# Optimization experiments

Measured on AMD Instinct MI355X. Metric: run time of the kernel, lower is better.

The kernel has to match this reference:

```python
import jax, jax.numpy as jnp
import numpy as np

N_NODES = 50000
N_EDGES = 400000
DIMS = [128, 256, 512, 256, 64, 2]


def setup_inputs() -> dict:
    key = jax.random.key(0)
    ks = jax.random.split(key, 16)
    x = jax.random.normal(ks[0], (N_NODES, DIMS[0]), dtype=jnp.float32)
    edge_index = jax.random.randint(ks[1], (2, N_EDGES), 0, N_NODES, dtype=jnp.int64)
    inp = {"x": x, "edge_index": edge_index}
    for i in range(5):
        fan_in, fan_out = DIMS[i], DIMS[i + 1]
        scale = (2.0 / (fan_in + fan_out)) ** 0.5  # glorot-ish
        inp[f"W{i+1}"] = jax.random.normal(ks[2 + 2 * i], (fan_in, fan_out), dtype=jnp.float32) * scale
        inp[f"b{i+1}"] = jnp.zeros((fan_out,), dtype=jnp.float32)
    return inp


def _gcn_norm(edge_index, n):
    # add self-loops, compute symmetric normalization D^{-1/2} A_hat D^{-1/2}
    loop = jnp.arange(n, dtype=edge_index.dtype)
    src = jnp.concatenate([edge_index[0], loop])
    dst = jnp.concatenate([edge_index[1], loop])
    deg = jax.ops.segment_sum(jnp.ones_like(dst, dtype=jnp.float32), dst, num_segments=n)
    dinv = jnp.where(deg > 0, jax.lax.rsqrt(deg), 0.0)
    norm = dinv[src] * dinv[dst]  # [E+N]
    return src, dst, norm


def _gcn_conv(h, W, b, src, dst, norm, n):
    h = h @ W                                   # [N, out]
    msg = h[src] * norm[:, None]                # gather + scale, [E+N, out]
    out = jax.ops.segment_sum(msg, dst, num_segments=n)  # scatter-add
    return out + b


def reference(x, edge_index, W1, b1, W2, b2, W3, b3, W4, b4, W5, b5):
    n = x.shape[0]
    src, dst, norm = _gcn_norm(edge_index, n)
    h = jax.nn.relu(_gcn_conv(x, W1, b1, src, dst, norm, n))
    h = jax.nn.relu(_gcn_conv(h, W2, b2, src, dst, norm, n))
    h = jax.nn.relu(_gcn_conv(h, W3, b3, src, dst, norm, n))
    h = jax.nn.relu(_gcn_conv(h, W4, b4, src, dst, norm, n))
    h = _gcn_conv(h, W5, b5, src, dst, norm, n)
    return jax.nn.log_softmax(h, axis=1)
```

## Files before the change

kernel.cpp:

```cpp
#include <hip/hip_runtime.h>
#include <math.h>

#define N_NODES 50000
#define N_EDGES 400000

typedef __bf16 bf16x8 __attribute__((ext_vector_type(8)));
typedef float f32x4 __attribute__((ext_vector_type(4)));

__device__ __forceinline__ unsigned bf16_rne(float v) {
    unsigned u = __float_as_uint(v);
    return (u + 0x7FFFu + ((u >> 16) & 1u)) >> 16;
}
__device__ __forceinline__ unsigned pack_split(float v) {
    unsigned hi = bf16_rne(v);
    float hif = __uint_as_float(hi << 16);
    unsigned lo = bf16_rne(v - hif);
    return (hi << 16) | lo;
}
__device__ __forceinline__ float unpack_ps(unsigned w) {
    return __uint_as_float(w & 0xFFFF0000u) + __uint_as_float(w << 16);
}

__global__ void k_zero_i(int* __restrict__ p, int n) {
    int i = blockIdx.x * blockDim.x + threadIdx.x;
    if (i < n) p[i] = 0;
}

__global__ void k_count(const int* __restrict__ dst, int* __restrict__ cnt) {
    int e = blockIdx.x * blockDim.x + threadIdx.x;
    if (e < N_EDGES) atomicAdd(&cnt[dst[e]], 1);
}

__global__ __launch_bounds__(1024) void k_scan(const int* __restrict__ cnt,
                                               int* __restrict__ rowptr,
                                               float* __restrict__ dinv, int n) {
    __shared__ int sm[1024];
    __shared__ int carry;
    if (threadIdx.x == 0) carry = 0;
    __syncthreads();
    for (int base = 0; base < n; base += 1024) {
        int i = base + threadIdx.x;
        int v = (i < n) ? cnt[i] : 0;
        sm[threadIdx.x] = v;
        __syncthreads();
        for (int off = 1; off < 1024; off <<= 1) {
            int t = (threadIdx.x >= (unsigned)off) ? sm[threadIdx.x - off] : 0;
            __syncthreads();
            sm[threadIdx.x] += t;
            __syncthreads();
        }
        if (i < n) {
            rowptr[i] = carry + sm[threadIdx.x] - v;
            dinv[i] = rsqrtf((float)(v + 1));
        }
        __syncthreads();
        if (threadIdx.x == 0) carry += sm[1023];
        __syncthreads();
    }
    if (threadIdx.x == 0) rowptr[n] = carry;
}

__global__ void k_copy_i(const int* __restrict__ s, int* __restrict__ d, int n) {
    int i = blockIdx.x * blockDim.x + threadIdx.x;
    if (i < n) d[i] = s[i];
}

__global__ void k_fill(const int* __restrict__ src, const int* __restrict__ dst,
                       int* __restrict__ cursor, int* __restrict__ csr) {
    int e = blockIdx.x * blockDim.x + threadIdx.x;
    if (e >= N_EDGES) return;
    int d = dst[e];
    int pos = atomicAdd(&cursor[d], 1);
    csr[pos] = src[e];
}

__global__ void k_wprep(const float* __restrict__ W, unsigned* __restrict__ Wtp, int K, int N) {
    int i = blockIdx.x * blockDim.x + threadIdx.x;
    if (i >= K * N) return;
    int k = i / N, n = i % N;
    Wtp[(size_t)n * K + k] = pack_split(W[i]);
}

__global__ void k_rowscale(const float* __restrict__ x, const float* __restrict__ dinv,
                           float* __restrict__ xs) {
    int idx = blockIdx.x * blockDim.x + threadIdx.x;
    if (idx >= N_NODES * 32) return;
    int i = idx >> 5;
    float4 v = ((const float4*)x)[idx];
    float s = dinv[i];
    v.x *= s; v.y *= s; v.z *= s; v.w *= s;
    ((float4*)xs)[idx] = v;
}

template <int VEC, int MODE, int INP, int OUTP>
__global__ __launch_bounds__(256) void k_agg(
    const void* __restrict__ gv, const int* __restrict__ rowptr,
    const int* __restrict__ csr, const float* __restrict__ dinv,
    const float* __restrict__ bias, void* __restrict__ ov)
{
    constexpr int W = 64 * VEC;
    const int wave = threadIdx.x >> 6, lane = threadIdx.x & 63;
    const int node = blockIdx.x * 4 + wave;
    if (node >= N_NODES) return;
    const int col = lane * VEC;

    float acc[VEC];
#pragma unroll
    for (int v = 0; v < VEC; ++v) acc[v] = 0.f;

    auto fetch_add = [&](int r) {
        if constexpr (INP) {
            const unsigned* p = (const unsigned*)gv + (size_t)r * W + col;
            if constexpr (VEC == 4) {
                uint4 t = *(const uint4*)p;
                acc[0] += unpack_ps(t.x); acc[1] += unpack_ps(t.y);
                acc[2] += unpack_ps(t.z); acc[3] += unpack_ps(t.w);
            } else if constexpr (VEC == 2) {
                uint2 t = *(const uint2*)p;
                acc[0] += unpack_ps(t.x); acc[1] += unpack_ps(t.y);
            } else acc[0] += unpack_ps(*p);
        } else {
            const float* p = (const float*)gv + (size_t)r * W + col;
            if constexpr (VEC == 4) {
                float4 t = *(const float4*)p;
                acc[0] += t.x; acc[1] += t.y; acc[2] += t.z; acc[3] += t.w;
            } else if constexpr (VEC == 2) {
                float2 t = *(const float2*)p;
                acc[0] += t.x; acc[1] += t.y;
            } else acc[0] += *(const float*)p;
        }
    };

    fetch_add(node);
    const int beg = rowptr[node], end = rowptr[node + 1];
    for (int j = beg; j < end; ++j) fetch_add(csr[j]);

    const float sc = dinv[node];
    float r[VEC];
#pragma unroll
    for (int v = 0; v < VEC; ++v) {
        float t = sc * acc[v];
        if (MODE == 1) t = fmaxf(t + bias[col + v], 0.f);
        r[v] = t;
    }
    if constexpr (OUTP) {
        unsigned* po = (unsigned*)ov + (size_t)node * W + col;
        if constexpr (VEC == 4)
            *(uint4*)po = make_uint4(pack_split(r[0]), pack_split(r[1]), pack_split(r[2]), pack_split(r[3]));
        else if constexpr (VEC == 2)
            *(uint2*)po = make_uint2(pack_split(r[0]), pack_split(r[1]));
        else *po = pack_split(r[0]);
    } else {
        float* po = (float*)ov + (size_t)node * W + col;
        if constexpr (VEC == 4) *(float4*)po = make_float4(r[0], r[1], r[2], r[3]);
        else if constexpr (VEC == 2) *(float2*)po = make_float2(r[0], r[1]);
        else *po = r[0];
    }
}

__global__ void k_agg2(const float* __restrict__ g, const int* __restrict__ rowptr,
                       const int* __restrict__ csr, const float* __restrict__ dinv,
                       float* __restrict__ o) {
    int i = blockIdx.x * blockDim.x + threadIdx.x;
    if (i >= N_NODES) return;
    float2 a = *(const float2*)&g[2 * (size_t)i];
    int beg = rowptr[i], end = rowptr[i + 1];
    for (int j = beg; j < end; ++j) {
        int s = csr[j];
        float2 t = *(const float2*)&g[2 * (size_t)s];
        a.x += t.x; a.y += t.y;
    }
    float sc = dinv[i];
    o[2 * (size_t)i + 0] = sc * a.x;
    o[2 * (size_t)i + 1] = sc * a.y;
}

__global__ __launch_bounds__(256) void k_gemm_mfma(
    const unsigned* __restrict__ Ap, const unsigned* __restrict__ Wtp,
    const float* __restrict__ dinv, const float* __restrict__ bias,
    unsigned* __restrict__ Gp, int M, int K, int N, int mode)
{
    __shared__ char lds[24576];
    char* Ahi = lds;
    char* Alo = lds + 8192;
    char* Bhi = lds + 16384;
    char* Blo = lds + 20480;

    const int tid = threadIdx.x;
    const int m0 = blockIdx.x * 128;
    const int n0 = blockIdx.y * 64;
    const int wv = tid >> 6, l = tid & 63;
    const int lr = l & 15, ls = l >> 4;

    int aoff[2], boff[4];
#pragma unroll
    for (int h = 0; h < 2; ++h) {
        int row = wv * 32 + h * 16 + lr;
        aoff[h] = (row * 64 + ls * 16) ^ ((row & 7) << 4);
    }
#pragma unroll
    for (int j = 0; j < 4; ++j) {
        int row = j * 16 + lr;
        boff[j] = (row * 64 + ls * 16) ^ ((row & 7) << 4);
    }

    f32x4 acc[2][4] = {};

    for (int kt = 0; kt < K; kt += 32) {
        __syncthreads();
#pragma unroll
        for (int p = 0; p < 4; ++p) {
            int c = p * 256 + tid;
            int row = c >> 3, c4 = (c & 7) * 4;
            int grow = m0 + row;
            uint4 w = make_uint4(0u, 0u, 0u, 0u);
            if (grow < M) w = *(const uint4*)&Ap[(size_t)grow * K + kt + c4];
            ushort4 hi, lo;
            hi.x = w.x >> 16; lo.x = w.x & 0xFFFFu;
            hi.y = w.y >> 16; lo.y = w.y & 0xFFFFu;
            hi.z = w.z >> 16; lo.z = w.z & 0xFFFFu;
            hi.w = w.w >> 16; lo.w = w.w & 0xFFFFu;
            int off = (row * 64 + c4 * 2) ^ ((row & 7) << 4);
            *(ushort4*)(Ahi + off) = hi;
            *(ushort4*)(Alo + off) = lo;
        }
#pragma unroll
        for (int p = 0; p < 2; ++p) {
            int c = p * 256 + tid;
            int row = c >> 3, c4 = (c & 7) * 4;
            uint4 w = *(const uint4*)&Wtp[(size_t)(n0 + row) * K + kt + c4];
            ushort4 hi, lo;
            hi.x = w.x >> 16; lo.x = w.x & 0xFFFFu;
            hi.y = w.y >> 16; lo.y = w.y & 0xFFFFu;
            hi.z = w.z >> 16; lo.z = w.z & 0xFFFFu;
            hi.w = w.w >> 16; lo.w = w.w & 0xFFFFu;
            int off = (row * 64 + c4 * 2) ^ ((row & 7) << 4);
            *(ushort4*)(Bhi + off) = hi;
            *(ushort4*)(Blo + off) = lo;
        }
        __syncthreads();

        bf16x8 ah[2], al[2], bh[4], bl[4];
#pragma unroll
        for (int h = 0; h < 2; ++h) {
            ah[h] = *(const bf16x8*)(Ahi + aoff[h]);
            al[h] = *(const bf16x8*)(Alo + aoff[h]);
        }
#pragma unroll
        for (int j = 0; j < 4; ++j) {
            bh[j] = *(const bf16x8*)(Bhi + boff[j]);
            bl[j] = *(const bf16x8*)(Blo + boff[j]);
        }
#pragma unroll
        for (int h = 0; h < 2; ++h)
#pragma unroll
            for (int j = 0; j < 4; ++j) {
                acc[h][j] = __builtin_amdgcn_mfma_f32_16x16x32_bf16(ah[h], bh[j], acc[h][j], 0, 0, 0);
                acc[h][j] = __builtin_amdgcn_mfma_f32_16x16x32_bf16(ah[h], bl[j], acc[h][j], 0, 0, 0);
                acc[h][j] = __builtin_amdgcn_mfma_f32_16x16x32_bf16(al[h], bh[j], acc[h][j], 0, 0, 0);
            }
    }

#pragma unroll
    for (int h = 0; h < 2; ++h)
#pragma unroll
        for (int j = 0; j < 4; ++j) {
            int col = n0 + j * 16 + lr;
            float bc = (mode >= 1) ? bias[col] : 0.f;
#pragma unroll
            for (int reg = 0; reg < 4; ++reg) {
                int r = m0 + wv * 32 + h * 16 + ls * 4 + reg;
                if (r < M) {
                    float t = acc[h][j][reg];
                    if (mode == 0)      t = dinv[r] * t;
                    else if (mode == 1) t = fmaxf(t + bc, 0.f);
                    else                t = dinv[r] * fmaxf(t + bc, 0.f);
                    Gp[(size_t)r * N + col] = pack_split(t);
                }
            }
        }
}

__global__ void k_gemm2(const float* __restrict__ A, const float* __restrict__ W,
                        const float* __restrict__ dinv, float* __restrict__ G, int M, int K)
{
    int i = blockIdx.x * blockDim.x + threadIdx.x;
    if (i >= M) return;
    float a0 = 0.f, a1 = 0.f;
    for (int k = 0; k < K; k += 4) {
        float4 a = *(const float4*)&A[(size_t)i * K + k];
        a0 += a.x * W[(k + 0) * 2 + 0] + a.y * W[(k + 1) * 2 + 0]
            + a.z * W[(k + 2) * 2 + 0] + a.w * W[(k + 3) * 2 + 0];
        a1 += a.x * W[(k + 0) * 2 + 1] + a.y * W[(k + 1) * 2 + 1]
            + a.z * W[(k + 2) * 2 + 1] + a.w * W[(k + 3) * 2 + 1];
    }
    float s = dinv[i];
    G[2 * (size_t)i + 0] = s * a0;
    G[2 * (size_t)i + 1] = s * a1;
}

__global__ void k_final(const float* __restrict__ lg, const float* __restrict__ bias,
                        float* __restrict__ out, int M)
{
    int i = blockIdx.x * blockDim.x + threadIdx.x;
    if (i >= M) return;
    float o0 = lg[2 * (size_t)i + 0] + bias[0];
    float o1 = lg[2 * (size_t)i + 1] + bias[1];
    float m = fmaxf(o0, o1);
    float lse = m + logf(expf(o0 - m) + expf(o1 - m));
    out[2 * (size_t)i + 0] = o0 - lse;
    out[2 * (size_t)i + 1] = o1 - lse;
}

extern "C" void kernel_launch(void* const* d_in, const int* in_sizes, int n_in,
                              void* d_out, int out_size, void* d_ws, size_t ws_size,
                              hipStream_t stream) {
    const float* x   = (const float*)d_in[0];
    const int*   ei  = (const int*)d_in[1];
    const int*   src = ei;
    const int*   dst = ei + N_EDGES;
    const float* W1 = (const float*)d_in[2];  const float* b1 = (const float*)d_in[3];
    const float* W2 = (const float*)d_in[4];  const float* b2 = (const float*)d_in[5];
    const float* W3 = (const float*)d_in[6];  const float* b3 = (const float*)d_in[7];
    const float* W4 = (const float*)d_in[8];  const float* b4 = (const float*)d_in[9];
    const float* W5 = (const float*)d_in[10]; const float* b5 = (const float*)d_in[11];
    float* out = (float*)d_out;

    char* ws = (char*)d_ws;
    float*    dinv   = (float*)(ws + 0);
    int*      cnt    = (int*)(ws + 256 * 1024);
    int*      rowptr = (int*)(ws + 512 * 1024);
    int*      cursor = (int*)(ws + 768 * 1024);
    int*      csr    = (int*)(ws + 1024 * 1024);
    unsigned* wt1 = (unsigned*)(ws + 3 * 1024 * 1024);
    unsigned* wt2 = wt1 + 128 * 256;
    unsigned* wt3 = wt2 + 256 * 512;
    unsigned* wt4 = wt3 + 512 * 256;

    char* D = ws + 6 * 1024 * 1024;
    float*    xs   = (float*)D;
    unsigned* aggx = (unsigned*)(D + (size_t)N_NODES * 128 * 4);
    unsigned* h1s  = (unsigned*)(D + (size_t)N_NODES * 512 * 4);
    unsigned* a2   = (unsigned*)(D + (size_t)N_NODES * 768 * 4);
    unsigned* h2   = (unsigned*)D;
    unsigned* g3s  = h1s;
    unsigned* h3   = a2;
    unsigned* g4s  = (unsigned*)D;
    float*    h4   = (float*)(D + (size_t)N_NODES * 64 * 4);
    float*    g5s  = (float*)(D + (size_t)N_NODES * 128 * 4);
    float*    lgt  = (float*)(D + (size_t)N_NODES * 132 * 4);

    const int T = 256;
    const int nodeB = (N_NODES + T - 1) / T;
    const int edgeB = (N_EDGES + T - 1) / T;
    const int aggB  = (N_NODES + 3) / 4;
    const int gx    = (N_NODES + 127) / 128;

    k_zero_i<<<nodeB, T, 0, stream>>>(cnt, N_NODES);
    k_count<<<edgeB, T, 0, stream>>>(dst, cnt);
    k_scan<<<1, 1024, 0, stream>>>(cnt, rowptr, dinv, N_NODES);
    k_copy_i<<<nodeB, T, 0, stream>>>(rowptr, cursor, N_NODES);
    k_fill<<<edgeB, T, 0, stream>>>(src, dst, cursor, csr);
    k_wprep<<<(128 * 256 + T - 1) / T, T, 0, stream>>>(W1, wt1, 128, 256);
    k_wprep<<<(256 * 512 + T - 1) / T, T, 0, stream>>>(W2, wt2, 256, 512);
    k_wprep<<<(512 * 256 + T - 1) / T, T, 0, stream>>>(W3, wt3, 512, 256);
    k_wprep<<<(256 * 64 + T - 1) / T, T, 0, stream>>>(W4, wt4, 256, 64);

    k_rowscale<<<(N_NODES * 32 + T - 1) / T, T, 0, stream>>>(x, dinv, xs);
    k_agg<2, 0, 0, 1><<<aggB, T, 0, stream>>>(xs, rowptr, csr, dinv, nullptr, aggx);
    k_gemm_mfma<<<dim3(gx, 4), T, 0, stream>>>(aggx, wt1, dinv, b1, h1s, N_NODES, 128, 256, 2);

    k_agg<4, 0, 1, 1><<<aggB, T, 0, stream>>>(h1s, rowptr, csr, dinv, nullptr, a2);
    k_gemm_mfma<<<dim3(gx, 8), T, 0, stream>>>(a2, wt2, dinv, b2, h2, N_NODES, 256, 512, 1);

    k_gemm_mfma<<<dim3(gx, 4), T, 0, stream>>>(h2, wt3, dinv, nullptr, g3s, N_NODES, 512, 256, 0);
    k_agg<4, 1, 1, 1><<<aggB, T, 0, stream>>>(g3s, rowptr, csr, dinv, b3, h3);

    k_gemm_mfma<<<dim3(gx, 1), T, 0, stream>>>(h3, wt4, dinv, nullptr, g4s, N_NODES, 256, 64, 0);
    k_agg<1, 1, 1, 0><<<aggB, T, 0, stream>>>(g4s, rowptr, csr, dinv, b4, h4);

    k_gemm2<<<nodeB, T, 0, stream>>>(h4, W5, dinv, g5s, N_NODES, 64);
    k_agg2<<<nodeB, T, 0, stream>>>(g5s, rowptr, csr, dinv, lgt);
    k_final<<<nodeB, T, 0, stream>>>(lgt, b5, out, N_NODES);
}
```

Measured before the change: 747.3 us.

## Template MFMA GEMM on 2x2 wave grid with larger N tiles

The split-bf16 MFMA GEMM becomes a template over per-wave tile sizes, and its four waves are arranged as a 2x2 grid instead of stacking along M. Blocks now cover 128x128 output tiles (128x64 for the last layer), which halves the number of blocks re-reading the A operand per row tile and raises arithmetic intensity per LDS load. The grid axes are swapped so column tiles vary fastest, letting blocks that share the same A rows run close together for L2 reuse. In exchange each wave holds more accumulators (4x4 fragments), which raises register pressure and may lower occupancy, and the larger tiles mean fewer blocks in flight.

```diff
diff --git a/kernel.cpp b/kernel.cpp
--- a/kernel.cpp
+++ b/kernel.cpp
@@ -175,43 +175,47 @@
     o[2 * (size_t)i + 1] = sc * a.y;
 }
 
+template <int WM, int WN>
 __global__ __launch_bounds__(256) void k_gemm_mfma(
     const unsigned* __restrict__ Ap, const unsigned* __restrict__ Wtp,
     const float* __restrict__ dinv, const float* __restrict__ bias,
     unsigned* __restrict__ Gp, int M, int K, int N, int mode)
 {
-    __shared__ char lds[24576];
+    constexpr int BM = 2 * WM, BN = 2 * WN;
+    constexpr int AF = WM / 16, BF = WN / 16;
+    __shared__ char lds[(2 * BM + 2 * BN) * 64];
     char* Ahi = lds;
-    char* Alo = lds + 8192;
-    char* Bhi = lds + 16384;
-    char* Blo = lds + 20480;
+    char* Alo = Ahi + BM * 64;
+    char* Bhi = Alo + BM * 64;
+    char* Blo = Bhi + BN * 64;
 
     const int tid = threadIdx.x;
-    const int m0 = blockIdx.x * 128;
-    const int n0 = blockIdx.y * 64;
+    const int m0 = blockIdx.y * BM;
+    const int n0 = blockIdx.x * BN;
     const int wv = tid >> 6, l = tid & 63;
+    const int wr = wv >> 1, wc = wv & 1;
     const int lr = l & 15, ls = l >> 4;
 
-    int aoff[2], boff[4];
-#pragma unroll
-    for (int h = 0; h < 2; ++h) {
-        int row = wv * 32 + h * 16 + lr;
-        aoff[h] = (row * 64 + ls * 16) ^ ((row & 7) << 4);
-    }
-#pragma unroll
-    for (int j = 0; j < 4; ++j) {
-        int row = j * 16 + lr;
+    int aoff[AF], boff[BF];
+#pragma unroll
+    for (int f = 0; f < AF; ++f) {
+        int row = wr * WM + f * 16 + lr;
+        aoff[f] = (row * 64 + ls * 16) ^ ((row & 7) << 4);
+    }
+#pragma unroll
+    for (int j = 0; j < BF; ++j) {
+        int row = wc * WN + j * 16 + lr;
         boff[j] = (row * 64 + ls * 16) ^ ((row & 7) << 4);
     }
 
-    f32x4 acc[2][4] = {};
+    f32x4 acc[AF][BF] = {};
 
     for (int kt = 0; kt < K; kt += 32) {
         __syncthreads();
 #pragma unroll
-        for (int p = 0; p < 4; ++p) {
+        for (int p = 0; p < BM / 32; ++p) {
             int c = p * 256 + tid;
-            int row = c >> 3, c4 = (c & 7) * 4;
+            int row = c >> 3, c4 = (c & 7) << 2;
             int grow = m0 + row;
             uint4 w = make_uint4(0u, 0u, 0u, 0u);
             if (grow < M) w = *(const uint4*)&Ap[(size_t)grow * K + kt + c4];
@@ -225,9 +229,9 @@
             *(ushort4*)(Alo + off) = lo;
         }
 #pragma unroll
-        for (int p = 0; p < 2; ++p) {
+        for (int p = 0; p < BN / 32; ++p) {
             int c = p * 256 + tid;
-            int row = c >> 3, c4 = (c & 7) * 4;
+            int row = c >> 3, c4 = (c & 7) << 2;
             uint4 w = *(const uint4*)&Wtp[(size_t)(n0 + row) * K + kt + c4];
             ushort4 hi, lo;
             hi.x = w.x >> 16; lo.x = w.x & 0xFFFFu;
@@ -240,38 +244,38 @@
         }
         __syncthreads();
 
-        bf16x8 ah[2], al[2], bh[4], bl[4];
-#pragma unroll
-        for (int h = 0; h < 2; ++h) {
-            ah[h] = *(const bf16x8*)(Ahi + aoff[h]);
-            al[h] = *(const bf16x8*)(Alo + aoff[h]);
-        }
-#pragma unroll
-        for (int j = 0; j < 4; ++j) {
+        bf16x8 ah[AF], al[AF], bh[BF], bl[BF];
+#pragma unroll
+        for (int f = 0; f < AF; ++f) {
+            ah[f] = *(const bf16x8*)(Ahi + aoff[f]);
+            al[f] = *(const bf16x8*)(Alo + aoff[f]);
+        }
+#pragma unroll
+        for (int j = 0; j < BF; ++j) {
             bh[j] = *(const bf16x8*)(Bhi + boff[j]);
             bl[j] = *(const bf16x8*)(Blo + boff[j]);
         }
 #pragma unroll
-        for (int h = 0; h < 2; ++h)
-#pragma unroll
-            for (int j = 0; j < 4; ++j) {
-                acc[h][j] = __builtin_amdgcn_mfma_f32_16x16x32_bf16(ah[h], bh[j], acc[h][j], 0, 0, 0);
-                acc[h][j] = __builtin_amdgcn_mfma_f32_16x16x32_bf16(ah[h], bl[j], acc[h][j], 0, 0, 0);
-                acc[h][j] = __builtin_amdgcn_mfma_f32_16x16x32_bf16(al[h], bh[j], acc[h][j], 0, 0, 0);
+        for (int f = 0; f < AF; ++f)
+#pragma unroll
+            for (int j = 0; j < BF; ++j) {
+                acc[f][j] = __builtin_amdgcn_mfma_f32_16x16x32_bf16(ah[f], bh[j], acc[f][j], 0, 0, 0);
+                acc[f][j] = __builtin_amdgcn_mfma_f32_16x16x32_bf16(ah[f], bl[j], acc[f][j], 0, 0, 0);
+                acc[f][j] = __builtin_amdgcn_mfma_f32_16x16x32_bf16(al[f], bh[j], acc[f][j], 0, 0, 0);
             }
     }
 
 #pragma unroll
-    for (int h = 0; h < 2; ++h)
-#pragma unroll
-        for (int j = 0; j < 4; ++j) {
-            int col = n0 + j * 16 + lr;
+    for (int f = 0; f < AF; ++f)
+#pragma unroll
+        for (int j = 0; j < BF; ++j) {
+            int col = n0 + wc * WN + j * 16 + lr;
             float bc = (mode >= 1) ? bias[col] : 0.f;
 #pragma unroll
             for (int reg = 0; reg < 4; ++reg) {
-                int r = m0 + wv * 32 + h * 16 + ls * 4 + reg;
+                int r = m0 + wr * WM + f * 16 + ls * 4 + reg;
                 if (r < M) {
-                    float t = acc[h][j][reg];
+                    float t = acc[f][j][reg];
                     if (mode == 0)      t = dinv[r] * t;
                     else if (mode == 1) t = fmaxf(t + bc, 0.f);
                     else                t = dinv[r] * fmaxf(t + bc, 0.f);
@@ -354,7 +358,7 @@
     const int nodeB = (N_NODES + T - 1) / T;
     const int edgeB = (N_EDGES + T - 1) / T;
     const int aggB  = (N_NODES + 3) / 4;
-    const int gx    = (N_NODES + 127) / 128;
+    const int gy    = (N_NODES + 127) / 128;
 
     k_zero_i<<<nodeB, T, 0, stream>>>(cnt, N_NODES);
     k_count<<<edgeB, T, 0, stream>>>(dst, cnt);
@@ -368,15 +372,15 @@
 
     k_rowscale<<<(N_NODES * 32 + T - 1) / T, T, 0, stream>>>(x, dinv, xs);
     k_agg<2, 0, 0, 1><<<aggB, T, 0, stream>>>(xs, rowptr, csr, dinv, nullptr, aggx);
-    k_gemm_mfma<<<dim3(gx, 4), T, 0, stream>>>(aggx, wt1, dinv, b1, h1s, N_NODES, 128, 256, 2);
+    k_gemm_mfma<64, 64><<<dim3(2, gy), T, 0, stream>>>(aggx, wt1, dinv, b1, h1s, N_NODES, 128, 256, 2);
 
     k_agg<4, 0, 1, 1><<<aggB, T, 0, stream>>>(h1s, rowptr, csr, dinv, nullptr, a2);
-    k_gemm_mfma<<<dim3(gx, 8), T, 0, stream>>>(a2, wt2, dinv, b2, h2, N_NODES, 256, 512, 1);
-
-    k_gemm_mfma<<<dim3(gx, 4), T, 0, stream>>>(h2, wt3, dinv, nullptr, g3s, N_NODES, 512, 256, 0);
+    k_gemm_mfma<64, 64><<<dim3(4, gy), T, 0, stream>>>(a2, wt2, dinv, b2, h2, N_NODES, 256, 512, 1);
+
+    k_gemm_mfma<64, 64><<<dim3(2, gy), T, 0, stream>>>(h2, wt3, dinv, nullptr, g3s, N_NODES, 512, 256, 0);
     k_agg<4, 1, 1, 1><<<aggB, T, 0, stream>>>(g3s, rowptr, csr, dinv, b3, h3);
 
-    k_gemm_mfma<<<dim3(gx, 1), T, 0, stream>>>(h3, wt4, dinv, nullptr, g4s, N_NODES, 256, 64, 0);
+    k_gemm_mfma<64, 32><<<dim3(1, gy), T, 0, stream>>>(h3, wt4, dinv, nullptr, g4s, N_NODES, 256, 64, 0);
     k_agg<1, 1, 1, 0><<<aggB, T, 0, stream>>>(g4s, rowptr, csr, dinv, b4, h4);
 
     k_gemm2<<<nodeB, T, 0, stream>>>(h4, W5, dinv, g5s, N_NODES, 64);
```

Measured after the change: 756.0 us. About the same (+1.2%).
